# Performance work log

Hardware: AMD Instinct MI355X
Metric: run time of the kernel (lower is better)

The kernel has to match this reference:

```python
import jax, jax.numpy as jnp
import numpy as np

DIM = 512
HEADS = 8
DIM_HEAD = 64
HIDDEN = HEADS * DIM_HEAD  # 512
B, C, H, W = 32, DIM, 32, 32


def setup_inputs() -> dict:
    key = jax.random.key(0)
    ks = jax.random.split(key, 7)
    s_in = 1.0 / np.sqrt(DIM)
    s_h = 1.0 / np.sqrt(HIDDEN)
    x = jax.random.normal(ks[0], (B, C, H, W), dtype=jnp.float32)
    Wq = jax.random.uniform(ks[1], (DIM, HIDDEN), jnp.float32, -s_in, s_in)
    Wk = jax.random.uniform(ks[2], (DIM, HIDDEN), jnp.float32, -s_in, s_in)
    Wv = jax.random.uniform(ks[3], (DIM, HIDDEN), jnp.float32, -s_in, s_in)
    Wp = jax.random.uniform(ks[4], (HIDDEN, DIM), jnp.float32, -s_h, s_h)
    bp = jax.random.uniform(ks[5], (DIM,), jnp.float32, -s_h, s_h)
    return {"x": x, "Wq": Wq, "Wk": Wk, "Wv": Wv, "Wp": Wp, "bp": bp}


def reference(x, Wq, Wk, Wv, Wp, bp):
    b, c, h, w = x.shape
    n = h * w
    xt = x.reshape(b, c, n).transpose(0, 2, 1)  # [B, N, C]
    q = (xt @ Wq).reshape(b, n, HEADS, DIM_HEAD)
    k = (xt @ Wk).reshape(b, n, HEADS, DIM_HEAD)
    v = (xt @ Wv).reshape(b, n, HEADS, DIM_HEAD)
    k_softmax = jax.nn.softmax(k, axis=1)  # softmax over tokens N
    context = jnp.einsum('bnhd,bnhv->bhdv', k_softmax, v)  # [B, H, D, D]
    out = jnp.einsum('bnhd,bhdv->bnhv', q, context).reshape(b, n, HIDDEN)
    out = out @ Wp + bp  # [B, N, C]
    return out.transpose(0, 2, 1).reshape(b, c, h, w)
```

## Files before the change

kernel.cpp:

```cpp
#include <hip/hip_runtime.h>
#include <hip/hip_bf16.h>


__device__ __forceinline__ float bf2f(unsigned short u) {
    union { unsigned int i; float f; } x;
    x.i = ((unsigned int)u) << 16;
    return x.f;
}
__device__ __forceinline__ unsigned short f2bf(float f) {
    unsigned int u = __float_as_uint(f);
    unsigned int lsb = (u >> 16) & 1u;
    u += 0x7fffu + lsb;
    return (unsigned short)(u >> 16);
}

__device__ __forceinline__ void glds16(const unsigned short* g, unsigned short* l) {
    __builtin_amdgcn_global_load_lds(
        (const __attribute__((address_space(1))) unsigned int*)g,
        (__attribute__((address_space(3))) unsigned int*)l,
        16, 0, 0);
}

typedef __bf16 bf16x8 __attribute__((ext_vector_type(8)));
typedef float  f32x4  __attribute__((ext_vector_type(4)));

__global__ void detect_dtype(const unsigned short* __restrict__ x, int* __restrict__ flag)
{
    int t = threadIdx.x;
    unsigned short u = x[2 * t];
    int e = (u >> 7) & 0xFF;
    int sane = (e >= 113 && e <= 142) ? 1 : 0;
    #pragma unroll
    for (int off = 32; off > 0; off >>= 1) sane += __shfl_xor(sane, off, 64);
    if (t == 0) *flag = (sane >= 32) ? 1 : 0;
}

__global__ __launch_bounds__(256) void transpose_x(
    const void* __restrict__ in, unsigned short* __restrict__ out,
    const int* __restrict__ flag)
{
    const int fl = *flag;
    const int b  = blockIdx.z;
    const int c0 = blockIdx.x * 64;
    const int r0 = blockIdx.y * 64;
    __shared__ unsigned short Ts[64][68];
    const int t   = threadIdx.x;
    const int tr  = t >> 4;
    const int tc4 = (t & 15) * 4;
    #pragma unroll
    for (int rr = 0; rr < 4; ++rr) {
        int rl = rr * 16 + tr;
        long off = (long)b * 524288 + (long)(r0 + rl) * 1024 + c0 + tc4;
        unsigned short v[4];
        if (fl) {
            ushort4 u = *(const ushort4*)((const unsigned short*)in + off);
            v[0] = u.x; v[1] = u.y; v[2] = u.z; v[3] = u.w;
        } else {
            float4 u = *(const float4*)((const float*)in + off);
            v[0] = f2bf(u.x); v[1] = f2bf(u.y); v[2] = f2bf(u.z); v[3] = f2bf(u.w);
        }
        #pragma unroll
        for (int q = 0; q < 4; ++q) Ts[tc4 + q][rl] = v[q];
    }
    __syncthreads();
    #pragma unroll
    for (int rr = 0; rr < 4; ++rr) {
        int cl = rr * 16 + tr;
        ushort4 o = *(const ushort4*)&Ts[cl][tc4];
        *(ushort4*)(out + (long)b * 524288 + (long)(c0 + cl) * 512 + r0 + tc4) = o;
    }
}

__global__ __launch_bounds__(256) void transpose_w3(
    const void* __restrict__ w0, const void* __restrict__ w1,
    const void* __restrict__ w2, unsigned short* __restrict__ out,
    unsigned short* __restrict__ wqb,
    const int* __restrict__ flag)
{
    const int fl = *flag;
    const int z  = blockIdx.z;
    const void* in = (z == 0) ? w0 : (z == 1) ? w1 : w2;
    unsigned short* op = out + (long)z * 262144;
    const int c0 = blockIdx.x * 64;
    const int r0 = blockIdx.y * 64;
    __shared__ unsigned short Ts[64][68];
    const int t   = threadIdx.x;
    const int tr  = t >> 4;
    const int tc4 = (t & 15) * 4;
    #pragma unroll
    for (int rr = 0; rr < 4; ++rr) {
        int rl = rr * 16 + tr;
        long off = (long)(r0 + rl) * 512 + c0 + tc4;
        unsigned short v[4];
        if (fl) {
            ushort4 u = *(const ushort4*)((const unsigned short*)in + off);
            v[0] = u.x; v[1] = u.y; v[2] = u.z; v[3] = u.w;
        } else {
            float4 u = *(const float4*)((const float*)in + off);
            v[0] = f2bf(u.x); v[1] = f2bf(u.y); v[2] = f2bf(u.z); v[3] = f2bf(u.w);
        }
        if (z == 0) {
            ushort4 s; s.x = v[0]; s.y = v[1]; s.z = v[2]; s.w = v[3];
            *(ushort4*)(wqb + off) = s;
        }
        #pragma unroll
        for (int q = 0; q < 4; ++q) Ts[tc4 + q][rl] = v[q];
    }
    __syncthreads();
    #pragma unroll
    for (int rr = 0; rr < 4; ++rr) {
        int cl = rr * 16 + tr;
        ushort4 o = *(const ushort4*)&Ts[cl][tc4];
        *(ushort4*)(op + (long)(c0 + cl) * 512 + r0 + tc4) = o;
    }
}

__global__ __launch_bounds__(512, 2) void gemm_bt_256(
    const unsigned short* __restrict__ A, long a_bstride,
    const unsigned short* __restrict__ Bm, long b_bstride,
    void* __restrict__ C, long c_bstride,
    const void* __restrict__ bias,
    int M, int N, int K, int mode,
    const int* __restrict__ flag)
{
    const int b  = blockIdx.z;
    const int n0 = blockIdx.x * 256;
    const int m0 = blockIdx.y * 256;
    const unsigned short* Ab = A  + (long)b * a_bstride;
    const unsigned short* Bb = Bm + (long)b * b_bstride;

    __shared__ unsigned short S[65536];

    const int t  = threadIdx.x;
    const int w  = t >> 6;
    const int l  = t & 63;
    const int fm = l & 15;
    const int kg = l >> 4;
    const int wr = w >> 2;
    const int wc = w & 3;

    const int rowb = w * 8 + (l >> 3);
    const int swz  = ((l & 7) ^ (l >> 3)) * 8;
    const unsigned short* gA = Ab + (long)(m0 + rowb) * K + swz;
    const unsigned short* gB = Bb + (long)(n0 + rowb) * K + swz;

    const int sA = fm & 7;

    f32x4 acc[8][4] = {};

    const int NT = K >> 6;

    auto STAGE = [&](int kt, int buf) {
        const long ko = (long)kt * 64;
        unsigned short* Ld = &S[buf * 32768];
        #pragma unroll
        for (int r = 0; r < 4; ++r)
            glds16(gA + (long)r * 64 * K + ko, Ld + r * 4096 + w * 512);
        #pragma unroll
        for (int r = 0; r < 4; ++r)
            glds16(gB + (long)r * 64 * K + ko, Ld + 16384 + r * 4096 + w * 512);
    };

    STAGE(0, 0);

    for (int tt = 0; tt < NT; ++tt) {
        if (tt + 1 < NT) {
            STAGE(tt + 1, (tt + 1) & 1);
            __builtin_amdgcn_sched_barrier(0);
            asm volatile("s_waitcnt vmcnt(8)" ::: "memory");
        } else {
            __builtin_amdgcn_sched_barrier(0);
            asm volatile("s_waitcnt vmcnt(0)" ::: "memory");
        }
        __builtin_amdgcn_sched_barrier(0);
        __builtin_amdgcn_s_barrier();
        __builtin_amdgcn_sched_barrier(0);

        {
            const unsigned short* Abuf = &S[(tt & 1) * 32768];
            const unsigned short* Bbuf = Abuf + 16384;
            bf16x8 bf[4][2];
            #pragma unroll
            for (int j = 0; j < 4; ++j)
                #pragma unroll
                for (int kk = 0; kk < 2; ++kk) {
                    const int row = wc * 64 + j * 16 + fm;
                    bf[j][kk] = *(const bf16x8*)&Bbuf[row * 64 + ((kk * 4 + kg) ^ sA) * 8];
                }
            #pragma unroll
            for (int q = 0; q < 4; ++q) {
                bf16x8 af[2][2];
                #pragma unroll
                for (int ii = 0; ii < 2; ++ii)
                    #pragma unroll
                    for (int kk = 0; kk < 2; ++kk) {
                        const int row = wr * 128 + (q * 2 + ii) * 16 + fm;
                        af[ii][kk] = *(const bf16x8*)&Abuf[row * 64 + ((kk * 4 + kg) ^ sA) * 8];
                    }
                __builtin_amdgcn_s_setprio(1);
                #pragma unroll
                for (int ii = 0; ii < 2; ++ii)
                    #pragma unroll
                    for (int j = 0; j < 4; ++j)
                        #pragma unroll
                        for (int kk = 0; kk < 2; ++kk)
                            acc[q * 2 + ii][j] = __builtin_amdgcn_mfma_f32_16x16x32_bf16(
                                bf[j][kk], af[ii][kk], acc[q * 2 + ii][j], 0, 0, 0);
                __builtin_amdgcn_s_setprio(0);
            }
        }

        __builtin_amdgcn_sched_barrier(0);
        __builtin_amdgcn_s_barrier();
        __builtin_amdgcn_sched_barrier(0);
    }

    const int fl = *flag;
    const long cb = (long)b * c_bstride;
    #pragma unroll
    for (int i = 0; i < 8; ++i) {
        const int m = m0 + wr * 128 + i * 16 + fm;
        float bv = 0.f;
        if (mode == 2 && bias)
            bv = fl ? bf2f(((const unsigned short*)bias)[m])
                    : ((const float*)bias)[m];
        #pragma unroll
        for (int j = 0; j < 4; ++j) {
            const int nb = n0 + wc * 64 + j * 16 + kg * 4;
            const long off = cb + (long)m * N + nb;
            if (mode == 0) {
                ushort4 o;
                o.x = f2bf(acc[i][j][0]); o.y = f2bf(acc[i][j][1]);
                o.z = f2bf(acc[i][j][2]); o.w = f2bf(acc[i][j][3]);
                *(ushort4*)&((unsigned short*)C)[off] = o;
            } else if (fl) {
                ushort4 o;
                o.x = f2bf(acc[i][j][0] + bv); o.y = f2bf(acc[i][j][1] + bv);
                o.z = f2bf(acc[i][j][2] + bv); o.w = f2bf(acc[i][j][3] + bv);
                *(ushort4*)&((unsigned short*)C)[off] = o;
            } else {
                float4 o;
                o.x = acc[i][j][0] + bv; o.y = acc[i][j][1] + bv;
                o.z = acc[i][j][2] + bv; o.w = acc[i][j][3] + bv;
                *(float4*)&((float*)C)[off] = o;
            }
        }
    }
}

__global__ __launch_bounds__(256) void gemm_bt_mfma(
    const unsigned short* __restrict__ A, long a_bstride,
    const unsigned short* __restrict__ Bm, long b_bstride,
    void* __restrict__ C, long c_bstride,
    const void* __restrict__ bias,
    int M, int N, int K, int mode,
    const int* __restrict__ flag)
{
    const int b  = blockIdx.z;
    const int n0 = blockIdx.x * 128;
    const int m0 = blockIdx.y * 128;
    const unsigned short* Ab = A  + (long)b * a_bstride;
    const unsigned short* Bb = Bm + (long)b * b_bstride;

    __shared__ unsigned short As[2 * 128 * 32];
    __shared__ unsigned short Bs[2 * 128 * 32];

    const int t    = threadIdx.x;
    const int w    = t >> 6;
    const int lane = t & 63;
    const int wm   = (w & 1) * 64;
    const int wn   = (w >> 1) * 64;
    const int fm   = lane & 15;
    const int kg   = lane >> 4;

    const int crow = lane >> 2;
    const int ccol = (lane & 3) * 8;

    f32x4 acc[4][4] = {};

    #pragma unroll
    for (int j = 0; j < 2; ++j) {
        const int chunk = w * 2 + j;
        const int row   = chunk * 16 + crow;
        glds16(Ab + (long)(m0 + row) * K + ccol, &As[chunk * 512]);
        glds16(Bb + (long)(n0 + row) * K + ccol, &Bs[chunk * 512]);
    }

    int cur = 0;
    for (int k0 = 0; k0 < K; k0 += 32) {
        __syncthreads();

        if (k0 + 32 < K) {
            const int kn  = k0 + 32;
            const int nxt = (cur ^ 1) * 4096;
            #pragma unroll
            for (int j = 0; j < 2; ++j) {
                const int chunk = w * 2 + j;
                const int row   = chunk * 16 + crow;
                glds16(Ab + (long)(m0 + row) * K + kn + ccol, &As[nxt + chunk * 512]);
                glds16(Bb + (long)(n0 + row) * K + kn + ccol, &Bs[nxt + chunk * 512]);
            }
        }

        const int bufo = cur * 4096;
        bf16x8 af[4], bf[4];
        #pragma unroll
        for (int i = 0; i < 4; ++i)
            af[i] = *(const bf16x8*)&As[bufo + (wm + i * 16 + fm) * 32 + kg * 8];
        #pragma unroll
        for (int j = 0; j < 4; ++j)
            bf[j] = *(const bf16x8*)&Bs[bufo + (wn + j * 16 + fm) * 32 + kg * 8];
        #pragma unroll
        for (int i = 0; i < 4; ++i)
            #pragma unroll
            for (int j = 0; j < 4; ++j)
                acc[i][j] = __builtin_amdgcn_mfma_f32_16x16x32_bf16(
                    bf[j], af[i], acc[i][j], 0, 0, 0);
        cur ^= 1;
    }

    const int fl = *flag;
    const long cb = (long)b * c_bstride;
    #pragma unroll
    for (int i = 0; i < 4; ++i) {
        const int m = m0 + wm + i * 16 + fm;
        float bv = 0.f;
        if (mode == 2 && bias)
            bv = fl ? bf2f(((const unsigned short*)bias)[m])
                    : ((const float*)bias)[m];
        #pragma unroll
        for (int j = 0; j < 4; ++j) {
            const int nb = n0 + wn + j * 16 + kg * 4;
            const long off = cb + (long)m * N + nb;
            if (mode == 0) {
                ushort4 o;
                o.x = f2bf(acc[i][j][0]); o.y = f2bf(acc[i][j][1]);
                o.z = f2bf(acc[i][j][2]); o.w = f2bf(acc[i][j][3]);
                *(ushort4*)&((unsigned short*)C)[off] = o;
            } else if (fl) {
                ushort4 o;
                o.x = f2bf(acc[i][j][0] + bv); o.y = f2bf(acc[i][j][1] + bv);
                o.z = f2bf(acc[i][j][2] + bv); o.w = f2bf(acc[i][j][3] + bv);
                *(ushort4*)&((unsigned short*)C)[off] = o;
            } else {
                float4 o;
                o.x = acc[i][j][0] + bv; o.y = acc[i][j][1] + bv;
                o.z = acc[i][j][2] + bv; o.w = acc[i][j][3] + bv;
                *(float4*)&((float*)C)[off] = o;
            }
        }
    }
}

__global__ __launch_bounds__(256) void ctx_softmax_mfma(
    const unsigned short* __restrict__ KV, float* __restrict__ ctx)
{
    const int bh = blockIdx.x;
    const unsigned short* Kb = KV + ((long)(bh >> 3) << 20) + (long)(bh & 7) * 65536;
    const unsigned short* Vb = Kb + 524288;

    const int t    = threadIdx.x;
    const int w    = t >> 6;
    const int lane = t & 63;
    const int fm   = lane & 15;
    const int kg   = lane >> 4;

    __shared__ float sm_m[64];
    __shared__ float sm_inv[64];

    {
        const int r = t >> 2;
        const int q = t & 3;
        const uint4* row = (const uint4*)(Kb + r * 1024 + q * 256);
        float mx = -3.402823466e+38f;
        #pragma unroll 8
        for (int i = 0; i < 32; ++i) {
            uint4 u = row[i];
            #pragma unroll
            for (int z = 0; z < 4; ++z) {
                unsigned int uu = ((const unsigned int*)&u)[z];
                float lo = bf2f((unsigned short)(uu & 0xffffu));
                float hi = bf2f((unsigned short)(uu >> 16));
                mx = fmaxf(mx, fmaxf(lo, hi));
            }
        }
        mx = fmaxf(mx, __shfl_xor(mx, 1, 64));
        mx = fmaxf(mx, __shfl_xor(mx, 2, 64));
        float s = 0.f;
        #pragma unroll 8
        for (int i = 0; i < 32; ++i) {
            uint4 u = row[i];
            #pragma unroll
            for (int z = 0; z < 4; ++z) {
                unsigned int uu = ((const unsigned int*)&u)[z];
                s += __expf(bf2f((unsigned short)(uu & 0xffffu)) - mx);
                s += __expf(bf2f((unsigned short)(uu >> 16)) - mx);
            }
        }
        s += __shfl_xor(s, 1, 64);
        s += __shfl_xor(s, 2, 64);
        if (q == 0) { sm_m[r] = mx; sm_inv[r] = 1.0f / s; }
    }
    __syncthreads();

    float rm[4], ri[4];
    #pragma unroll
    for (int i = 0; i < 4; ++i) {
        rm[i] = sm_m[i * 16 + fm];
        ri[i] = sm_inv[i * 16 + fm];
    }

    f32x4 acc[4][4] = {};

    #pragma unroll 2
    for (int c = 0; c < 8; ++c) {
        const int k0 = w * 256 + c * 32;
        bf16x8 af[4], bf[4];
        #pragma unroll
        for (int i = 0; i < 4; ++i) {
            uint4 u = *(const uint4*)(Kb + (long)(i * 16 + fm) * 1024 + k0 + kg * 8);
            unsigned short o[8];
            #pragma unroll
            for (int z = 0; z < 4; ++z) {
                unsigned int uu = ((const unsigned int*)&u)[z];
                float lo = __expf(bf2f((unsigned short)(uu & 0xffffu)) - rm[i]) * ri[i];
                float hi = __expf(bf2f((unsigned short)(uu >> 16))     - rm[i]) * ri[i];
                o[2 * z]     = f2bf(lo);
                o[2 * z + 1] = f2bf(hi);
            }
            af[i] = *(const bf16x8*)o;
        }
        #pragma unroll
        for (int j = 0; j < 4; ++j)
            bf[j] = *(const bf16x8*)(Vb + (long)(j * 16 + fm) * 1024 + k0 + kg * 8);
        #pragma unroll
        for (int i = 0; i < 4; ++i)
            #pragma unroll
            for (int j = 0; j < 4; ++j)
                acc[i][j] = __builtin_amdgcn_mfma_f32_16x16x32_bf16(
                    af[i], bf[j], acc[i][j], 0, 0, 0);
    }

    __shared__ float red[64][65];
    for (int ph = 0; ph < 4; ++ph) {
        if (w == ph) {
            #pragma unroll
            for (int i = 0; i < 4; ++i)
                #pragma unroll
                for (int j = 0; j < 4; ++j)
                    #pragma unroll
                    for (int r = 0; r < 4; ++r) {
                        const int m = i * 16 + kg * 4 + r;
                        const int n = j * 16 + fm;
                        if (ph == 0) red[m][n]  = acc[i][j][r];
                        else         red[m][n] += acc[i][j][r];
                    }
        }
        __syncthreads();
    }
    float* cp = ctx + (long)bh * 4096;
    for (int i = t; i < 4096; i += 256) cp[i] = red[i >> 6][i & 63];
}

__global__ __launch_bounds__(256) void weff_kernel(
    const float* __restrict__ ctx,
    const void* __restrict__ Wp,
    unsigned short* __restrict__ WeffT,
    const int* __restrict__ flag)
{
    const int fl = *flag;
    const int c0 = blockIdx.x * 64;
    const int h  = blockIdx.y;
    const int b  = blockIdx.z;

    __shared__ float Cs[64][65];
    __shared__ float Ws[64][68];

    const int t = threadIdx.x;
    const int tx = t & 15, ty = t >> 4;

    const float* cb = ctx + ((long)b * 8 + h) * 4096;
    for (int i = t; i < 4096; i += 256) Cs[i >> 6][i & 63] = cb[i];
    for (int i = t; i < 4096; i += 256) {
        int v = i >> 6, c = i & 63;
        long idx = (long)(h * 64 + v) * 512 + c0 + c;
        Ws[v][c] = fl ? bf2f(((const unsigned short*)Wp)[idx])
                      : ((const float*)Wp)[idx];
    }
    __syncthreads();

    float acc[4][4];
    #pragma unroll
    for (int i = 0; i < 4; ++i)
        #pragma unroll
        for (int j = 0; j < 4; ++j) acc[i][j] = 0.f;

    #pragma unroll
    for (int v = 0; v < 64; ++v) {
        float a[4], d[4];
        #pragma unroll
        for (int i = 0; i < 4; ++i) a[i] = Ws[v][ty * 4 + i];
        #pragma unroll
        for (int j = 0; j < 4; ++j) d[j] = Cs[tx * 4 + j][v];
        #pragma unroll
        for (int i = 0; i < 4; ++i)
            #pragma unroll
            for (int j = 0; j < 4; ++j) acc[i][j] += a[i] * d[j];
    }
    #pragma unroll
    for (int i = 0; i < 4; ++i) {
        ushort4 o;
        o.x = f2bf(acc[i][0]); o.y = f2bf(acc[i][1]);
        o.z = f2bf(acc[i][2]); o.w = f2bf(acc[i][3]);
        *(ushort4*)&WeffT[((long)b * 512 + c0 + ty * 4 + i) * 512 + h * 64 + tx * 4] = o;
    }
}

extern "C" void kernel_launch(void* const* d_in, const int* in_sizes, int n_in,
                              void* d_out, int out_size, void* d_ws, size_t ws_size,
                              hipStream_t stream) {
    const void* x  = d_in[0];
    const void* Wq = d_in[1];
    const void* Wk = d_in[2];
    const void* Wv = d_in[3];
    const void* Wp = d_in[4];
    const void* bp = d_in[5];

    char* ws = (char*)d_ws;
    unsigned short* Xt    = (unsigned short*)(ws);
    unsigned short* KV    = (unsigned short*)(ws + 33554432ll);
    unsigned short* Ft    = (unsigned short*)(ws + 33554432ll);
    float*          ctx   = (float*)(ws + 100663296ll);
    unsigned short* WeffT = (unsigned short*)(ws + 104857600ll);
    unsigned short* WT    = (unsigned short*)(ws + 121634816ll);
    unsigned short* Wqb   = (unsigned short*)(ws + 123207680ll);
    int*            flag  = (int*)(ws + 123731968ll);

    detect_dtype<<<dim3(1), dim3(64), 0, stream>>>((const unsigned short*)x, flag);

    transpose_x<<<dim3(16, 8, 32), 256, 0, stream>>>(x, Xt, flag);
    transpose_w3<<<dim3(8, 8, 3), 256, 0, stream>>>(Wq, Wk, Wv, WT, Wqb, flag);

    const long XB = 1024ll * 512;
    gemm_bt_256<<<dim3(4, 4, 32), 512, 0, stream>>>(
        WT + 262144, 0, Xt, XB, KV, 1048576ll, nullptr, 1024, 1024, 512, 0, flag);

    ctx_softmax_mfma<<<dim3(256), 256, 0, stream>>>(KV, ctx);

    weff_kernel<<<dim3(8, 8, 32), 256, 0, stream>>>(ctx, Wp, WeffT, flag);

    gemm_bt_mfma<<<dim3(4, 4, 32), 256, 0, stream>>>(
        WeffT, 262144ll, Wqb, 0, Ft, 262144ll, nullptr, 512, 512, 512, 0, flag);

    gemm_bt_256<<<dim3(4, 2, 32), 512, 0, stream>>>(
        Ft, 262144ll, Xt, XB, d_out, 524288ll, bp, 512, 1024, 512, 2, flag);
}
```

Baseline: 300.1 us.

## Interleave next-tile global-to-LDS prefetch with MFMA phases in GEMM main loop

Restructures the double-buffered GEMM K-loop so the prefetch of the next tile's B and A slices is issued inside the first two of four compute phases instead of all at once before compute. Each phase loads A fragments from LDS, optionally issues part of the prefetch, synchronises, then runs MFMAs. The aim is to spread memory traffic across the compute so issue slots contend less. In exchange it adds a workgroup barrier per phase and a full vmcnt(0) wait at the end of each iteration, which may add synchronisation stalls.

```diff
diff --git a/kernel.cpp b/kernel.cpp
--- a/kernel.cpp
+++ b/kernel.cpp
@@ -150,69 +150,88 @@
 
     const int NT = K >> 6;
 
-    auto STAGE = [&](int kt, int buf) {
-        const long ko = (long)kt * 64;
-        unsigned short* Ld = &S[buf * 32768];
+    {
+        unsigned short* Ld = &S[0];
         #pragma unroll
         for (int r = 0; r < 4; ++r)
-            glds16(gA + (long)r * 64 * K + ko, Ld + r * 4096 + w * 512);
+            glds16(gB + (long)r * 64 * K, Ld + 16384 + r * 4096 + w * 512);
         #pragma unroll
         for (int r = 0; r < 4; ++r)
-            glds16(gB + (long)r * 64 * K + ko, Ld + 16384 + r * 4096 + w * 512);
-    };
-
-    STAGE(0, 0);
+            glds16(gA + (long)r * 64 * K, Ld + r * 4096 + w * 512);
+    }
+    __builtin_amdgcn_sched_barrier(0);
+    asm volatile("s_waitcnt vmcnt(0)" ::: "memory");
+    __builtin_amdgcn_sched_barrier(0);
+    __builtin_amdgcn_s_barrier();
+    __builtin_amdgcn_sched_barrier(0);
 
     for (int tt = 0; tt < NT; ++tt) {
-        if (tt + 1 < NT) {
-            STAGE(tt + 1, (tt + 1) & 1);
-            __builtin_amdgcn_sched_barrier(0);
-            asm volatile("s_waitcnt vmcnt(8)" ::: "memory");
-        } else {
-            __builtin_amdgcn_sched_barrier(0);
-            asm volatile("s_waitcnt vmcnt(0)" ::: "memory");
-        }
-        __builtin_amdgcn_sched_barrier(0);
-        __builtin_amdgcn_s_barrier();
-        __builtin_amdgcn_sched_barrier(0);
-
-        {
-            const unsigned short* Abuf = &S[(tt & 1) * 32768];
-            const unsigned short* Bbuf = Abuf + 16384;
-            bf16x8 bf[4][2];
-            #pragma unroll
-            for (int j = 0; j < 4; ++j)
+        const unsigned short* Abuf = &S[(tt & 1) * 32768];
+        const unsigned short* Bbuf = Abuf + 16384;
+        unsigned short* Ln = &S[((tt + 1) & 1) * 32768];
+        const bool pre = (tt + 1 < NT);
+        const long ko = (long)(tt + 1) * 64;
+
+        bf16x8 bf[4][2];
+
+        #pragma unroll
+        for (int p = 0; p < 4; ++p) {
+            if (p == 0) {
+                #pragma unroll
+                for (int j = 0; j < 4; ++j)
+                    #pragma unroll
+                    for (int kk = 0; kk < 2; ++kk) {
+                        const int row = wc * 64 + j * 16 + fm;
+                        bf[j][kk] = *(const bf16x8*)&Bbuf[row * 64 + ((kk * 4 + kg) ^ sA) * 8];
+                    }
+            }
+            bf16x8 af[2][2];
+            #pragma unroll
+            for (int ii = 0; ii < 2; ++ii)
                 #pragma unroll
                 for (int kk = 0; kk < 2; ++kk) {
-                    const int row = wc * 64 + j * 16 + fm;
-                    bf[j][kk] = *(const bf16x8*)&Bbuf[row * 64 + ((kk * 4 + kg) ^ sA) * 8];
+                    const int row = wr * 128 + (p * 2 + ii) * 16 + fm;
+                    af[ii][kk] = *(const bf16x8*)&Abuf[row * 64 + ((kk * 4 + kg) ^ sA) * 8];
                 }
-            #pragma unroll
-            for (int q = 0; q < 4; ++q) {
-                bf16x8 af[2][2];
+
+            if (pre && p == 0) {
                 #pragma unroll
-                for (int ii = 0; ii < 2; ++ii)
+                for (int r = 0; r < 4; ++r)
+                    glds16(gB + (long)r * 64 * K + ko, Ln + 16384 + r * 4096 + w * 512);
+            }
+            if (pre && p == 1) {
+                #pragma unroll
+                for (int r = 0; r < 4; ++r)
+                    glds16(gA + (long)r * 64 * K + ko, Ln + r * 4096 + w * 512);
+            }
+
+            __builtin_amdgcn_sched_barrier(0);
+            __builtin_amdgcn_s_barrier();
+            asm volatile("s_waitcnt lgkmcnt(0)" ::: "memory");
+            __builtin_amdgcn_sched_barrier(0);
+
+            __builtin_amdgcn_s_setprio(1);
+            #pragma unroll
+            for (int ii = 0; ii < 2; ++ii)
+                #pragma unroll
+                for (int j = 0; j < 4; ++j)
                     #pragma unroll
-                    for (int kk = 0; kk < 2; ++kk) {
-                        const int row = wr * 128 + (q * 2 + ii) * 16 + fm;
-                        af[ii][kk] = *(const bf16x8*)&Abuf[row * 64 + ((kk * 4 + kg) ^ sA) * 8];
-                    }
-                __builtin_amdgcn_s_setprio(1);
-                #pragma unroll
-                for (int ii = 0; ii < 2; ++ii)
-                    #pragma unroll
-                    for (int j = 0; j < 4; ++j)
-                        #pragma unroll
-                        for (int kk = 0; kk < 2; ++kk)
-                            acc[q * 2 + ii][j] = __builtin_amdgcn_mfma_f32_16x16x32_bf16(
-                                bf[j][kk], af[ii][kk], acc[q * 2 + ii][j], 0, 0, 0);
-                __builtin_amdgcn_s_setprio(0);
-            }
-        }
-
-        __builtin_amdgcn_sched_barrier(0);
-        __builtin_amdgcn_s_barrier();
-        __builtin_amdgcn_sched_barrier(0);
+                    for (int kk = 0; kk < 2; ++kk)
+                        acc[p * 2 + ii][j] = __builtin_amdgcn_mfma_f32_16x16x32_bf16(
+                            bf[j][kk], af[ii][kk], acc[p * 2 + ii][j], 0, 0, 0);
+            __builtin_amdgcn_s_setprio(0);
+
+            __builtin_amdgcn_sched_barrier(0);
+            __builtin_amdgcn_s_barrier();
+            __builtin_amdgcn_sched_barrier(0);
+        }
+
+        if (pre) {
+            asm volatile("s_waitcnt vmcnt(0)" ::: "memory");
+            __builtin_amdgcn_sched_barrier(0);
+            __builtin_amdgcn_s_barrier();
+            __builtin_amdgcn_sched_barrier(0);
+        }
     }
 
     const int fl = *flag;
```

New measurement: 299.5 us. About the same (-0.2%).
